# Kernel tuning notes

Measured on AMD Instinct MI355X. Metric: run time of the kernel, lower is better.

The kernel has to match this reference:

```python
import jax, jax.numpy as jnp
import numpy as np

TAU = 1.0
EPS = 1e-30
LN_EPS = 1e-5


def setup_inputs() -> dict:
    key = jax.random.key(0)
    ks = jax.random.split(key, 5)
    N, E, D_in, D_out = 50000, 800000, 128, 128
    x = jax.random.normal(ks[0], (N, D_in), dtype=jnp.float32)
    edge_src = jax.random.randint(ks[1], (E,), 0, N, dtype=jnp.int64)
    edge_dst = jax.random.randint(ks[2], (E,), 0, N, dtype=jnp.int64)
    W = jax.random.normal(ks[3], (2 * D_in, D_out), dtype=jnp.float32) * (1.0 / np.sqrt(2 * D_in))
    b = jnp.zeros((D_out,), dtype=jnp.float32)
    gamma = jnp.ones((D_out,), dtype=jnp.float32)
    beta = jnp.zeros((D_out,), dtype=jnp.float32)
    return {"x": x, "edge_src": edge_src, "edge_dst": edge_dst, "W": W, "b": b, "gamma": gamma, "beta": beta}


def _scatter_logsumexp(src, index, dim_size):
    # src: [E, D] gathered neighbor features, index: [E] target node ids
    scaled = src.astype(jnp.float32) / TAU
    mx = jax.ops.segment_max(scaled, index, num_segments=dim_size)  # [N, D], -inf for empty
    exp_val = jnp.exp(scaled - mx[index])                            # [E, D]
    sum_exp = jax.ops.segment_sum(exp_val, index, num_segments=dim_size)  # [N, D]
    out = TAU * (mx + jnp.log(jnp.maximum(sum_exp, EPS)))
    deg = jax.ops.segment_sum(jnp.ones_like(index, dtype=jnp.int32), index, num_segments=dim_size)
    return jnp.where((deg > 0)[:, None], out, 0.0)


def reference(x, edge_src, edge_dst, W, b, gamma, beta):
    N = x.shape[0]
    src_feat = x[edge_src]                                  # [E, D] gather
    agg = _scatter_logsumexp(src_feat, edge_dst, N)         # [N, D]
    h = jnp.concatenate([x, agg], axis=-1) @ W + b          # [N, D_out]
    mean = jnp.mean(h, axis=-1, keepdims=True)
    var = jnp.var(h, axis=-1, keepdims=True)
    h = (h - mean) * jax.lax.rsqrt(var + LN_EPS) * gamma + beta
    return jax.nn.relu(h)
```

## Files before the change

### kernel.cpp

```cpp
#include <hip/hip_runtime.h>
#include <math.h>

#define D 128
#define EPS 1e-30f
#define LN_EPS 1e-5f

#define BINSHIFT 9
#define BINW 512
#define NBIN_MAX 128
#define P1_EPB 4096

typedef long long ll;
typedef __attribute__((ext_vector_type(8))) short short8;
typedef __attribute__((ext_vector_type(4))) float f32x4;

__device__ inline unsigned short f2bf(float f) {
    unsigned int u = __float_as_uint(f);
    u += 0x7FFF + ((u >> 16) & 1);
    return (unsigned short)(u >> 16);
}

__device__ inline float bf2f_lo(unsigned int w) { return __uint_as_float(w << 16); }
__device__ inline float bf2f_hi(unsigned int w) { return __uint_as_float(w & 0xFFFF0000u); }

__device__ inline bool idx_is_i64(const void* p, int n_nodes) {
    const ll* q = (const ll*)p;
    bool ok = true;
#pragma unroll
    for (int i = 0; i < 4; ++i) {
        ll v = q[i];
        if (v < 0 || v >= (ll)n_nodes) ok = false;
    }
    return ok;
}

__device__ inline int load_idx(const void* p, ll e, bool is64) {
    return is64 ? (int)((const ll*)p)[e] : ((const int*)p)[e];
}


__global__ __launch_bounds__(256) void k_prep(const float* __restrict__ x,
                                              unsigned short* __restrict__ A, int N) {
    int i = blockIdx.x * 256 + threadIdx.x;
    if (i >= N * 32) return;
    int n = i >> 5, c4 = i & 31;
    float4 v = *(const float4*)(x + (ll)n * D + c4 * 4);
    ushort4 o;
    o.x = f2bf(v.x); o.y = f2bf(v.y); o.z = f2bf(v.z); o.w = f2bf(v.w);
    *(ushort4*)(A + (ll)n * 256 + c4 * 4) = o;
}

__global__ __launch_bounds__(256) void k_wt(const float* __restrict__ W,
                                            unsigned short* __restrict__ WT) {
    int idx = blockIdx.x * 256 + threadIdx.x;
    int k = idx >> 7, n = idx & 127;
    WT[n * 256 + k] = f2bf(W[idx]);
}

__global__ __launch_bounds__(256) void k_pass1a(const void* __restrict__ edst,
                                                int* __restrict__ bincnt, int E, int N) {
    __shared__ int hist[NBIN_MAX];
    bool is64 = idx_is_i64(edst, N);
    int t = threadIdx.x;
    if (t < NBIN_MAX) hist[t] = 0;
    __syncthreads();
    ll base = (ll)blockIdx.x * P1_EPB;
    int cnt = (int)min((ll)P1_EPB, (ll)E - base);
    for (int i = t; i < cnt; i += 256) {
        int d = load_idx(edst, base + i, is64);
        atomicAdd(&hist[d >> BINSHIFT], 1);
    }
    __syncthreads();
    if (t < NBIN_MAX && hist[t]) atomicAdd(&bincnt[t], hist[t]);
}

__global__ __launch_bounds__(NBIN_MAX) void k_binscan(const int* __restrict__ bincnt,
                                                      int* __restrict__ pbase,
                                                      int* __restrict__ pcur,
                                                      int* __restrict__ off, int E, int N) {
    __shared__ int s[NBIN_MAX];
    int t = threadIdx.x;
    int v = bincnt[t];
    s[t] = v;
    __syncthreads();
    for (int o = 1; o < NBIN_MAX; o <<= 1) {
        int xv = (t >= o) ? s[t - o] : 0;
        __syncthreads();
        s[t] += xv;
        __syncthreads();
    }
    pbase[t] = s[t] - v;
    pcur[t]  = s[t] - v;
    if (t == NBIN_MAX - 1) { pbase[NBIN_MAX] = s[t]; off[N] = E; }
}

__global__ __launch_bounds__(256) void k_pass1b(const void* __restrict__ esrc,
                                                const void* __restrict__ edst,
                                                int* __restrict__ pcur,
                                                unsigned int* __restrict__ pairs,
                                                int E, int N) {
    __shared__ unsigned int sp[P1_EPB];
    __shared__ int hist[NBIN_MAX];
    __shared__ int curs[NBIN_MAX];
    bool is64s = idx_is_i64(esrc, N);
    bool is64d = idx_is_i64(edst, N);
    int t = threadIdx.x;
    if (t < NBIN_MAX) hist[t] = 0;
    __syncthreads();
    ll base = (ll)blockIdx.x * P1_EPB;
    int cnt = (int)min((ll)P1_EPB, (ll)E - base);
    for (int i = t; i < cnt; i += 256) {
        unsigned int s = (unsigned int)load_idx(esrc, base + i, is64s);
        unsigned int d = (unsigned int)load_idx(edst, base + i, is64d);
        sp[i] = (d << 16) | s;
        atomicAdd(&hist[d >> BINSHIFT], 1);
    }
    __syncthreads();
    if (t < NBIN_MAX) curs[t] = hist[t] ? atomicAdd(&pcur[t], hist[t]) : 0;
    __syncthreads();
    for (int i = t; i < cnt; i += 256) {
        unsigned int p = sp[i];
        int b = p >> (16 + BINSHIFT);
        int pos = atomicAdd(&curs[b], 1);
        pairs[pos] = p;
    }
}

__global__ __launch_bounds__(256) void k_pass2(const unsigned int* __restrict__ pairs,
                                               const int* __restrict__ pbase,
                                               int* __restrict__ off,
                                               unsigned short* __restrict__ bucket, int N) {
    __shared__ int dhist[BINW];
    __shared__ int dcur[BINW];
    __shared__ int ssum[256];
    int b = blockIdx.x, t = threadIdx.x;
    int p0 = pbase[b], p1 = pbase[b + 1];
    int n0 = b << BINSHIFT;
    for (int j = t; j < BINW; j += 256) dhist[j] = 0;
    __syncthreads();
    for (int i = p0 + t; i < p1; i += 256)
        atomicAdd(&dhist[(pairs[i] >> 16) & (BINW - 1)], 1);
    __syncthreads();
    int h0 = dhist[2 * t], h1 = dhist[2 * t + 1];
    int loc = h0 + h1;
    ssum[t] = loc;
    __syncthreads();
    for (int o = 1; o < 256; o <<= 1) {
        int xv = (t >= o) ? ssum[t - o] : 0;
        __syncthreads();
        ssum[t] += xv;
        __syncthreads();
    }
    int ex = ssum[t] - loc;
    dcur[2 * t]     = ex;
    dcur[2 * t + 1] = ex + h0;
    __syncthreads();
    int lim = min(BINW, N - n0);
    for (int j = t; j < lim; j += 256) off[n0 + j] = p0 + dcur[j];
    __syncthreads();
    for (int i = p0 + t; i < p1; i += 256) {
        unsigned int p = pairs[i];
        int dl = (p >> 16) & (BINW - 1);
        int pos = p0 + atomicAdd(&dcur[dl], 1);
        bucket[pos] = (unsigned short)(p & 0xFFFFu);
    }
}

__global__ __launch_bounds__(256) void k_aggregate(const int* __restrict__ off,
                                                   const unsigned short* __restrict__ bucket,
                                                   unsigned short* __restrict__ A, int N) {
    int w = threadIdx.x >> 6, lane = threadIdx.x & 63;
    int n = blockIdx.x * 4 + w;
    if (n >= N) return;
    int start = off[n], end = off[n + 1];
    int sub = lane >> 4, c16 = lane & 15;
    float acc[8];
#pragma unroll
    for (int j = 0; j < 8; ++j) acc[j] = 0.f;
    for (int e = start + sub; e < end; e += 4) {
        int src = bucket[e];
        uint4 v = *(const uint4*)(A + (ll)src * 256 + c16 * 8);
        acc[0] += __expf(bf2f_lo(v.x)); acc[1] += __expf(bf2f_hi(v.x));
        acc[2] += __expf(bf2f_lo(v.y)); acc[3] += __expf(bf2f_hi(v.y));
        acc[4] += __expf(bf2f_lo(v.z)); acc[5] += __expf(bf2f_hi(v.z));
        acc[6] += __expf(bf2f_lo(v.w)); acc[7] += __expf(bf2f_hi(v.w));
    }
#pragma unroll
    for (int j = 0; j < 8; ++j) {
        acc[j] += __shfl_xor(acc[j], 16, 64);
        acc[j] += __shfl_xor(acc[j], 32, 64);
    }
    if (sub == 0) {
        int dg = end - start;
        unsigned int o[4];
#pragma unroll
        for (int k = 0; k < 4; ++k) {
            float a0 = (dg > 0) ? __logf(fmaxf(acc[2 * k],     EPS)) : 0.f;
            float a1 = (dg > 0) ? __logf(fmaxf(acc[2 * k + 1], EPS)) : 0.f;
            o[k] = (unsigned int)f2bf(a0) | ((unsigned int)f2bf(a1) << 16);
        }
        *(uint4*)(A + (ll)n * 256 + 128 + c16 * 8) = make_uint4(o[0], o[1], o[2], o[3]);
    }
}

__global__ __launch_bounds__(256) void k_gemm_mfma(
        const unsigned short* __restrict__ A,
        const unsigned short* __restrict__ WT,
        const float* __restrict__ bias,
        const float* __restrict__ gamma,
        const float* __restrict__ beta,
        float* __restrict__ out, int N) {
    __shared__ unsigned char sA[64 * 512];
    __shared__ float2 sPart[2][64];
    int t = threadIdx.x;
    int l = t & 63, w = t >> 6;
    int wr = w >> 1, wc = w & 1;
    int n0 = blockIdx.x * 64;

    const uint4* gA = (const uint4*)(A + (ll)n0 * 256);
#pragma unroll
    for (int i = 0; i < 8; ++i) {
        int c = i * 256 + t;
        int row = c >> 5, cc = c & 31;
        uint4 v = make_uint4(0u, 0u, 0u, 0u);
        if (n0 + row < N) v = gA[row * 32 + cc];
        *(uint4*)(sA + row * 512 + ((cc * 16) ^ ((row & 7) << 4))) = v;
    }
    __syncthreads();

    f32x4 acc[2][4];
#pragma unroll
    for (int m = 0; m < 2; ++m)
#pragma unroll
        for (int n = 0; n < 4; ++n) acc[m][n] = (f32x4){0.f, 0.f, 0.f, 0.f};

    const int lr = l & 15, lk = l >> 4;
    const int aswz = (lr & 7) << 4;
    const unsigned short* wbase = WT + (wc * 64 + lr) * 256 + lk * 8;

#pragma unroll
    for (int ks = 0; ks < 8; ++ks) {
        short8 a[2], b[4];
#pragma unroll
        for (int m = 0; m < 2; ++m) {
            int arow = wr * 32 + m * 16 + lr;
            a[m] = *(const short8*)(sA + arow * 512 + ((ks * 64 + lk * 16) ^ aswz));
        }
#pragma unroll
        for (int n = 0; n < 4; ++n)
            b[n] = *(const short8*)(wbase + n * 16 * 256 + ks * 32);
#pragma unroll
        for (int m = 0; m < 2; ++m)
#pragma unroll
            for (int n = 0; n < 4; ++n)
                acc[m][n] = __builtin_amdgcn_mfma_f32_16x16x32_bf16(a[m], b[n], acc[m][n], 0, 0, 0);
    }

    const int col_base = wc * 64 + lr;
    float bn[4], gn[4], ben[4];
#pragma unroll
    for (int n = 0; n < 4; ++n) {
        int col = col_base + n * 16;
        bn[n] = bias[col]; gn[n] = gamma[col]; ben[n] = beta[col];
    }
#pragma unroll
    for (int m = 0; m < 2; ++m) {
#pragma unroll
        for (int r = 0; r < 4; ++r) {
            float s = 0.f, q = 0.f;
#pragma unroll
            for (int n = 0; n < 4; ++n) {
                float v = acc[m][n][r] + bn[n];
                acc[m][n][r] = v;
                s += v; q += v * v;
            }
#pragma unroll
            for (int o = 1; o < 16; o <<= 1) {
                s += __shfl_xor(s, o, 64);
                q += __shfl_xor(q, o, 64);
            }
            if (lr == 0) {
                int rowl = wr * 32 + m * 16 + lk * 4 + r;
                sPart[wc][rowl] = make_float2(s, q);
            }
        }
    }
    __syncthreads();
#pragma unroll
    for (int m = 0; m < 2; ++m) {
#pragma unroll
        for (int r = 0; r < 4; ++r) {
            int rowl = wr * 32 + m * 16 + lk * 4 + r;
            float2 p0 = sPart[0][rowl], p1 = sPart[1][rowl];
            float ssum = p0.x + p1.x, qsum = p0.y + p1.y;
            float mean = ssum * (1.f / 128.f);
            float var  = qsum * (1.f / 128.f) - mean * mean;
            float rstd = rsqrtf(var + LN_EPS);
            int grow = n0 + rowl;
            if (grow < N) {
                float* op = out + (ll)grow * 128;
#pragma unroll
                for (int n = 0; n < 4; ++n) {
                    float y = (acc[m][n][r] - mean) * rstd * gn[n] + ben[n];
                    op[col_base + n * 16] = fmaxf(y, 0.f);
                }
            }
        }
    }
}


__global__ __launch_bounds__(256) void k_hist(const void* __restrict__ edst,
                                              int* __restrict__ deg, int E, int N) {
    bool is64 = idx_is_i64(edst, N);
    int i = blockIdx.x * 256 + threadIdx.x;
    if (i < E) atomicAdd(&deg[load_idx(edst, i, is64)], 1);
}

__global__ __launch_bounds__(256) void k_scanA(const int* __restrict__ deg,
                                               int* __restrict__ off,
                                               int* __restrict__ bsum, int N) {
    __shared__ int s[256];
    int b = blockIdx.x, t = threadIdx.x;
    int base = b * 1024 + t * 4;
    int v0 = 0, v1 = 0, v2 = 0, v3 = 0;
    if (base + 0 < N) v0 = deg[base + 0];
    if (base + 1 < N) v1 = deg[base + 1];
    if (base + 2 < N) v2 = deg[base + 2];
    if (base + 3 < N) v3 = deg[base + 3];
    int loc = v0 + v1 + v2 + v3;
    s[t] = loc;
    __syncthreads();
    for (int o = 1; o < 256; o <<= 1) {
        int xv = (t >= o) ? s[t - o] : 0;
        __syncthreads();
        s[t] += xv;
        __syncthreads();
    }
    int run = s[t] - loc;
    if (t == 255) bsum[b] = s[255];
    if (base + 0 < N) off[base + 0] = run; run += v0;
    if (base + 1 < N) off[base + 1] = run; run += v1;
    if (base + 2 < N) off[base + 2] = run; run += v2;
    if (base + 3 < N) off[base + 3] = run;
}

__global__ __launch_bounds__(256) void k_scanB(const int* __restrict__ bsum,
                                               int* __restrict__ bbase, int NB) {
    __shared__ int s[256];
    int t = threadIdx.x;
    int v = (t < NB) ? bsum[t] : 0;
    s[t] = v;
    __syncthreads();
    for (int o = 1; o < 256; o <<= 1) {
        int xv = (t >= o) ? s[t - o] : 0;
        __syncthreads();
        s[t] += xv;
        __syncthreads();
    }
    if (t < NB) bbase[t] = s[t] - v;
}

__global__ __launch_bounds__(256) void k_scanC(int* __restrict__ off,
                                               int* __restrict__ cur,
                                               const int* __restrict__ bbase, int N, int E) {
    int b = blockIdx.x, t = threadIdx.x;
    int add = bbase[b];
    int base = b * 1024 + t * 4;
#pragma unroll
    for (int i = 0; i < 4; ++i) {
        int idx = base + i;
        if (idx < N) {
            int o = off[idx] + add;
            off[idx] = o;
            cur[idx] = o;
        }
    }
    if (b == 0 && t == 0) off[N] = E;
}

__global__ __launch_bounds__(256) void k_scatter32(const void* __restrict__ esrc,
                                                   const void* __restrict__ edst,
                                                   int* __restrict__ cur,
                                                   unsigned short* __restrict__ bucket,
                                                   int E, int N) {
    bool is64s = idx_is_i64(esrc, N);
    bool is64d = idx_is_i64(edst, N);
    int i = blockIdx.x * 256 + threadIdx.x;
    if (i < E) {
        int s = load_idx(esrc, i, is64s);
        int d = load_idx(edst, i, is64d);
        int pos = atomicAdd(&cur[d], 1);
        bucket[pos] = (unsigned short)s;
    }
}


__global__ __launch_bounds__(256) void scatter_expsum(
        const float* __restrict__ x, const void* __restrict__ esrc_raw,
        const void* __restrict__ edst_raw, float* __restrict__ sumexp,
        int* __restrict__ deg, int E, int N) {
    ll tid = (ll)blockIdx.x * blockDim.x + threadIdx.x;
    ll total = (ll)E * 32;
    if (tid >= total) return;
    bool is64 = idx_is_i64(esrc_raw, N);
    ll e = tid >> 5;
    int q = (int)(tid & 31);
    int s = load_idx(esrc_raw, e, is64);
    int d = load_idx(edst_raw, e, is64);
    const float4 v = *reinterpret_cast<const float4*>(x + (ll)s * D + q * 4);
    float* outp = sumexp + (ll)d * D + q * 4;
    atomicAdd(outp + 0, expf(v.x));
    atomicAdd(outp + 1, expf(v.y));
    atomicAdd(outp + 2, expf(v.z));
    atomicAdd(outp + 3, expf(v.w));
    if (q == 0) atomicAdd(deg + d, 1);
}

__global__ __launch_bounds__(128) void gemm_ln_relu_fb(
        const float* __restrict__ x, const float* __restrict__ sumexp,
        const int* __restrict__ deg, const float* __restrict__ W,
        const float* __restrict__ bias, const float* __restrict__ gamma,
        const float* __restrict__ beta, float* __restrict__ out) {
    const int n = blockIdx.x;
    const int t = threadIdx.x;
    __shared__ float v[2 * D];
    __shared__ float s_sum[2], s_sq[2];
    v[t] = x[(ll)n * D + t];
    float se = sumexp[(ll)n * D + t];
    v[D + t] = (deg[n] > 0) ? logf(fmaxf(se, EPS)) : 0.0f;
    __syncthreads();
    float acc = bias[t];
#pragma unroll 8
    for (int k = 0; k < 2 * D; ++k) acc += v[k] * W[k * D + t];
    float sum = acc, sq = acc * acc;
#pragma unroll
    for (int o = 32; o > 0; o >>= 1) {
        sum += __shfl_xor(sum, o, 64);
        sq  += __shfl_xor(sq, o, 64);
    }
    int w = t >> 6;
    if ((t & 63) == 0) { s_sum[w] = sum; s_sq[w] = sq; }
    __syncthreads();
    float mean = (s_sum[0] + s_sum[1]) * (1.0f / D);
    float var  = (s_sq[0] + s_sq[1]) * (1.0f / D) - mean * mean;
    float r = rsqrtf(var + LN_EPS);
    float y = (acc - mean) * r * gamma[t] + beta[t];
    out[(ll)n * D + t] = fmaxf(y, 0.0f);
}

__global__ __launch_bounds__(128) void k_aggregate_mid(const float* __restrict__ x,
                                                       const unsigned short* __restrict__ bucket,
                                                       const int* __restrict__ off,
                                                       unsigned short* __restrict__ A, int N) {
    int n = blockIdx.x, t = threadIdx.x;
    int start = __builtin_amdgcn_readfirstlane(off[n]);
    int end   = __builtin_amdgcn_readfirstlane(off[n + 1]);
    float acc = 0.f;
    for (int e = start; e < end; ++e) {
        int s0 = bucket[e];
        acc += __expf(x[(ll)s0 * D + t]);
    }
    float agg = (end > start) ? __logf(fmaxf(acc, EPS)) : 0.f;
    A[(ll)n * 256 + t]       = f2bf(x[(ll)n * D + t]);
    A[(ll)n * 256 + 128 + t] = f2bf(agg);
}


extern "C" void kernel_launch(void* const* d_in, const int* in_sizes, int n_in,
                              void* d_out, int out_size, void* d_ws, size_t ws_size,
                              hipStream_t stream) {
    const float* x     = (const float*)d_in[0];
    const void*  esrc  = d_in[1];
    const void*  edst  = d_in[2];
    const float* W     = (const float*)d_in[3];
    const float* bias  = (const float*)d_in[4];
    const float* gamma = (const float*)d_in[5];
    const float* beta  = (const float*)d_in[6];

    const int E = in_sizes[1];
    const int N = in_sizes[0] / D;
    float* out = (float*)d_out;
    unsigned short* A = (unsigned short*)d_out;

    size_t need_fast = ((size_t)(N + 1) + 128 + 129 + 128 + (size_t)E) * 4
                     + (size_t)E * 2 + 2 + 65536;
    const int NB = (N + 1023) / 1024;
    size_t need_mid = ((size_t)3 * N + 1 + 512 + 16384) * 4 + (size_t)E * 2 + 2;

    if (N <= 65536 && ws_size >= need_fast) {
        int* off            = (int*)d_ws;
        int* bincnt         = off + (N + 1);
        int* pbase          = bincnt + 128;
        int* pcur           = pbase + 129;
        unsigned int* pairs = (unsigned int*)(pcur + 128);
        unsigned short* bucket = (unsigned short*)(pairs + E);
        unsigned short* wt  = (unsigned short*)((char*)(bucket + E) + (((size_t)(bucket + E)) & 2 ? 2 : 0));

        const int NBIN = (N + BINW - 1) >> BINSHIFT;
        const int EB = (E + P1_EPB - 1) / P1_EPB;

        hipMemsetAsync(bincnt, 0, 128 * sizeof(int), stream);
        k_prep<<<(N * 32 + 255) / 256, 256, 0, stream>>>(x, A, N);
        k_wt<<<128, 256, 0, stream>>>(W, wt);
        k_pass1a<<<EB, 256, 0, stream>>>(edst, bincnt, E, N);
        k_binscan<<<1, NBIN_MAX, 0, stream>>>(bincnt, pbase, pcur, off, E, N);
        k_pass1b<<<EB, 256, 0, stream>>>(esrc, edst, pcur, pairs, E, N);
        k_pass2<<<NBIN, 256, 0, stream>>>(pairs, pbase, off, bucket, N);
        k_aggregate<<<(N + 3) / 4, 256, 0, stream>>>(off, bucket, A, N);
        k_gemm_mfma<<<(N + 63) / 64, 256, 0, stream>>>(A, wt, bias, gamma, beta, out, N);
    } else if (N <= 65536 && ws_size >= need_mid && NB <= 256) {
        int* deg    = (int*)d_ws;
        int* off    = deg + N;
        int* cur    = off + (N + 1);
        int* bsum   = cur + N;
        int* bbase  = bsum + 256;
        unsigned short* wt = (unsigned short*)(bbase + 256);
        unsigned short* bucket = wt + 32768;

        hipMemsetAsync(deg, 0, (size_t)N * sizeof(int), stream);
        int eb = (E + 255) / 256;
        k_wt<<<128, 256, 0, stream>>>(W, wt);
        k_hist<<<eb, 256, 0, stream>>>(edst, deg, E, N);
        k_scanA<<<NB, 256, 0, stream>>>(deg, off, bsum, N);
        k_scanB<<<1, 256, 0, stream>>>(bsum, bbase, NB);
        k_scanC<<<NB, 256, 0, stream>>>(off, cur, bbase, N, E);
        k_scatter32<<<eb, 256, 0, stream>>>(esrc, edst, cur, bucket, E, N);
        k_aggregate_mid<<<N, 128, 0, stream>>>(x, bucket, off, A, N);
        k_gemm_mfma<<<(N + 63) / 64, 256, 0, stream>>>(A, wt, bias, gamma, beta, out, N);
    } else {
        float* sumexp = out;
        int* deg = (int*)d_ws;
        hipMemsetAsync(sumexp, 0, (size_t)N * D * sizeof(float), stream);
        hipMemsetAsync(deg, 0, (size_t)N * sizeof(int), stream);
        ll total = (ll)E * 32;
        int blocks = (int)((total + 255) / 256);
        scatter_expsum<<<blocks, 256, 0, stream>>>(x, esrc, edst, sumexp, deg, E, N);
        gemm_ln_relu_fb<<<N, D, 0, stream>>>(x, sumexp, deg, W, bias, gamma, beta, out);
    }
}
```

Before: 136.0 us.

## Fuse prep, weight transpose and bin histogram into one setup kernel; unroll aggregation

Merges the x-to-bf16 conversion, the W transpose and the per-block destination-bin histogram into a single launch. The histogram now writes per-block counts that k_binscan sums, which removes the memset and the global atomics. The aggregation loop is also unrolled by two so that two gathers are in flight at once. This cuts launch overhead and adds latency hiding, at the cost of a serial loop over EB rows inside the single-block binscan.

```diff
diff --git a/kernel.cpp b/kernel.cpp
--- a/kernel.cpp
+++ b/kernel.cpp
@@ -39,48 +39,55 @@
 }
 
 
-__global__ __launch_bounds__(256) void k_prep(const float* __restrict__ x,
-                                              unsigned short* __restrict__ A, int N) {
-    int i = blockIdx.x * 256 + threadIdx.x;
-    if (i >= N * 32) return;
-    int n = i >> 5, c4 = i & 31;
-    float4 v = *(const float4*)(x + (ll)n * D + c4 * 4);
-    ushort4 o;
-    o.x = f2bf(v.x); o.y = f2bf(v.y); o.z = f2bf(v.z); o.w = f2bf(v.w);
-    *(ushort4*)(A + (ll)n * 256 + c4 * 4) = o;
-}
-
-__global__ __launch_bounds__(256) void k_wt(const float* __restrict__ W,
-                                            unsigned short* __restrict__ WT) {
-    int idx = blockIdx.x * 256 + threadIdx.x;
-    int k = idx >> 7, n = idx & 127;
-    WT[n * 256 + k] = f2bf(W[idx]);
-}
-
-__global__ __launch_bounds__(256) void k_pass1a(const void* __restrict__ edst,
-                                                int* __restrict__ bincnt, int E, int N) {
+__global__ __launch_bounds__(256) void k_setup(const float* __restrict__ x,
+                                               unsigned short* __restrict__ A,
+                                               const float* __restrict__ W,
+                                               unsigned short* __restrict__ WT,
+                                               const void* __restrict__ edst,
+                                               int* __restrict__ bhist,
+                                               int N, int E, int PREP_B, int WT_B) {
     __shared__ int hist[NBIN_MAX];
+    int b = blockIdx.x, t = threadIdx.x;
+    if (b < PREP_B) {
+        int i = b * 256 + t;
+        if (i < N * 32) {
+            int n = i >> 5, c4 = i & 31;
+            float4 v = *(const float4*)(x + (ll)n * D + c4 * 4);
+            ushort4 o;
+            o.x = f2bf(v.x); o.y = f2bf(v.y); o.z = f2bf(v.z); o.w = f2bf(v.w);
+            *(ushort4*)(A + (ll)n * 256 + c4 * 4) = o;
+        }
+        return;
+    }
+    b -= PREP_B;
+    if (b < WT_B) {
+        int idx = b * 256 + t;
+        int k = idx >> 7, n = idx & 127;
+        WT[n * 256 + k] = f2bf(W[idx]);
+        return;
+    }
+    b -= WT_B;
+    if (t < NBIN_MAX) hist[t] = 0;
+    __syncthreads();
     bool is64 = idx_is_i64(edst, N);
-    int t = threadIdx.x;
-    if (t < NBIN_MAX) hist[t] = 0;
-    __syncthreads();
-    ll base = (ll)blockIdx.x * P1_EPB;
+    ll base = (ll)b * P1_EPB;
     int cnt = (int)min((ll)P1_EPB, (ll)E - base);
     for (int i = t; i < cnt; i += 256) {
         int d = load_idx(edst, base + i, is64);
         atomicAdd(&hist[d >> BINSHIFT], 1);
     }
     __syncthreads();
-    if (t < NBIN_MAX && hist[t]) atomicAdd(&bincnt[t], hist[t]);
-}
-
-__global__ __launch_bounds__(NBIN_MAX) void k_binscan(const int* __restrict__ bincnt,
+    if (t < NBIN_MAX) bhist[b * NBIN_MAX + t] = hist[t];
+}
+
+__global__ __launch_bounds__(NBIN_MAX) void k_binscan(const int* __restrict__ bhist, int EB,
                                                       int* __restrict__ pbase,
                                                       int* __restrict__ pcur,
                                                       int* __restrict__ off, int E, int N) {
     __shared__ int s[NBIN_MAX];
     int t = threadIdx.x;
-    int v = bincnt[t];
+    int v = 0;
+    for (int i = 0; i < EB; ++i) v += bhist[i * NBIN_MAX + t];
     s[t] = v;
     __syncthreads();
     for (int o = 1; o < NBIN_MAX; o <<= 1) {
@@ -174,16 +181,32 @@
     if (n >= N) return;
     int start = off[n], end = off[n + 1];
     int sub = lane >> 4, c16 = lane & 15;
+    const uint4* A4 = (const uint4*)A;
     float acc[8];
 #pragma unroll
     for (int j = 0; j < 8; ++j) acc[j] = 0.f;
-    for (int e = start + sub; e < end; e += 4) {
-        int src = bucket[e];
-        uint4 v = *(const uint4*)(A + (ll)src * 256 + c16 * 8);
-        acc[0] += __expf(bf2f_lo(v.x)); acc[1] += __expf(bf2f_hi(v.x));
-        acc[2] += __expf(bf2f_lo(v.y)); acc[3] += __expf(bf2f_hi(v.y));
-        acc[4] += __expf(bf2f_lo(v.z)); acc[5] += __expf(bf2f_hi(v.z));
-        acc[6] += __expf(bf2f_lo(v.w)); acc[7] += __expf(bf2f_hi(v.w));
+    int e = start + sub;
+    for (; e + 4 < end; e += 8) {
+        int s0 = bucket[e];
+        int s1 = bucket[e + 4];
+        uint4 v0 = A4[(ll)s0 * 32 + c16];
+        uint4 v1 = A4[(ll)s1 * 32 + c16];
+        acc[0] += __expf(bf2f_lo(v0.x)); acc[1] += __expf(bf2f_hi(v0.x));
+        acc[2] += __expf(bf2f_lo(v0.y)); acc[3] += __expf(bf2f_hi(v0.y));
+        acc[4] += __expf(bf2f_lo(v0.z)); acc[5] += __expf(bf2f_hi(v0.z));
+        acc[6] += __expf(bf2f_lo(v0.w)); acc[7] += __expf(bf2f_hi(v0.w));
+        acc[0] += __expf(bf2f_lo(v1.x)); acc[1] += __expf(bf2f_hi(v1.x));
+        acc[2] += __expf(bf2f_lo(v1.y)); acc[3] += __expf(bf2f_hi(v1.y));
+        acc[4] += __expf(bf2f_lo(v1.z)); acc[5] += __expf(bf2f_hi(v1.z));
+        acc[6] += __expf(bf2f_lo(v1.w)); acc[7] += __expf(bf2f_hi(v1.w));
+    }
+    if (e < end) {
+        int s0 = bucket[e];
+        uint4 v0 = A4[(ll)s0 * 32 + c16];
+        acc[0] += __expf(bf2f_lo(v0.x)); acc[1] += __expf(bf2f_hi(v0.x));
+        acc[2] += __expf(bf2f_lo(v0.y)); acc[3] += __expf(bf2f_hi(v0.y));
+        acc[4] += __expf(bf2f_lo(v0.z)); acc[5] += __expf(bf2f_hi(v0.z));
+        acc[6] += __expf(bf2f_lo(v0.w)); acc[7] += __expf(bf2f_hi(v0.w));
     }
 #pragma unroll
     for (int j = 0; j < 8; ++j) {
@@ -310,6 +333,13 @@
 }
 
 
+__global__ __launch_bounds__(256) void k_wt(const float* __restrict__ W,
+                                            unsigned short* __restrict__ WT) {
+    int idx = blockIdx.x * 256 + threadIdx.x;
+    int k = idx >> 7, n = idx & 127;
+    WT[n * 256 + k] = f2bf(W[idx]);
+}
+
 __global__ __launch_bounds__(256) void k_hist(const void* __restrict__ edst,
                                               int* __restrict__ deg, int E, int N) {
     bool is64 = idx_is_i64(edst, N);
@@ -393,6 +423,23 @@
         int pos = atomicAdd(&cur[d], 1);
         bucket[pos] = (unsigned short)s;
     }
+}
+
+__global__ __launch_bounds__(128) void k_aggregate_mid(const float* __restrict__ x,
+                                                       const unsigned short* __restrict__ bucket,
+                                                       const int* __restrict__ off,
+                                                       unsigned short* __restrict__ A, int N) {
+    int n = blockIdx.x, t = threadIdx.x;
+    int start = __builtin_amdgcn_readfirstlane(off[n]);
+    int end   = __builtin_amdgcn_readfirstlane(off[n + 1]);
+    float acc = 0.f;
+    for (int e = start; e < end; ++e) {
+        int s0 = bucket[e];
+        acc += __expf(x[(ll)s0 * D + t]);
+    }
+    float agg = (end > start) ? __logf(fmaxf(acc, EPS)) : 0.f;
+    A[(ll)n * 256 + t]       = f2bf(x[(ll)n * D + t]);
+    A[(ll)n * 256 + 128 + t] = f2bf(agg);
 }
 
 
@@ -449,23 +496,6 @@
     out[(ll)n * D + t] = fmaxf(y, 0.0f);
 }
 
-__global__ __launch_bounds__(128) void k_aggregate_mid(const float* __restrict__ x,
-                                                       const unsigned short* __restrict__ bucket,
-                                                       const int* __restrict__ off,
-                                                       unsigned short* __restrict__ A, int N) {
-    int n = blockIdx.x, t = threadIdx.x;
-    int start = __builtin_amdgcn_readfirstlane(off[n]);
-    int end   = __builtin_amdgcn_readfirstlane(off[n + 1]);
-    float acc = 0.f;
-    for (int e = start; e < end; ++e) {
-        int s0 = bucket[e];
-        acc += __expf(x[(ll)s0 * D + t]);
-    }
-    float agg = (end > start) ? __logf(fmaxf(acc, EPS)) : 0.f;
-    A[(ll)n * 256 + t]       = f2bf(x[(ll)n * D + t]);
-    A[(ll)n * 256 + 128 + t] = f2bf(agg);
-}
-
 
 extern "C" void kernel_launch(void* const* d_in, const int* in_sizes, int n_in,
                               void* d_out, int out_size, void* d_ws, size_t ws_size,
@@ -483,28 +513,26 @@
     float* out = (float*)d_out;
     unsigned short* A = (unsigned short*)d_out;
 
-    size_t need_fast = ((size_t)(N + 1) + 128 + 129 + 128 + (size_t)E) * 4
+    const int EB = (E + P1_EPB - 1) / P1_EPB;
+    const int PREP_B = (N * 32 + 255) / 256;
+    const int NBIN = (N + BINW - 1) >> BINSHIFT;
+
+    size_t need_fast = ((size_t)(N + 1) + 129 + 128 + (size_t)EB * NBIN_MAX + (size_t)E) * 4
                      + (size_t)E * 2 + 2 + 65536;
     const int NB = (N + 1023) / 1024;
     size_t need_mid = ((size_t)3 * N + 1 + 512 + 16384) * 4 + (size_t)E * 2 + 2;
 
     if (N <= 65536 && ws_size >= need_fast) {
         int* off            = (int*)d_ws;
-        int* bincnt         = off + (N + 1);
-        int* pbase          = bincnt + 128;
+        int* pbase          = off + (N + 1);
         int* pcur           = pbase + 129;
-        unsigned int* pairs = (unsigned int*)(pcur + 128);
+        int* bhist          = pcur + 128;
+        unsigned int* pairs = (unsigned int*)(bhist + (size_t)EB * NBIN_MAX);
         unsigned short* bucket = (unsigned short*)(pairs + E);
         unsigned short* wt  = (unsigned short*)((char*)(bucket + E) + (((size_t)(bucket + E)) & 2 ? 2 : 0));
 
-        const int NBIN = (N + BINW - 1) >> BINSHIFT;
-        const int EB = (E + P1_EPB - 1) / P1_EPB;
-
-        hipMemsetAsync(bincnt, 0, 128 * sizeof(int), stream);
-        k_prep<<<(N * 32 + 255) / 256, 256, 0, stream>>>(x, A, N);
-        k_wt<<<128, 256, 0, stream>>>(W, wt);
-        k_pass1a<<<EB, 256, 0, stream>>>(edst, bincnt, E, N);
-        k_binscan<<<1, NBIN_MAX, 0, stream>>>(bincnt, pbase, pcur, off, E, N);
+        k_setup<<<PREP_B + 128 + EB, 256, 0, stream>>>(x, A, W, wt, edst, bhist, N, E, PREP_B, 128);
+        k_binscan<<<1, NBIN_MAX, 0, stream>>>(bhist, EB, pbase, pcur, off, E, N);
         k_pass1b<<<EB, 256, 0, stream>>>(esrc, edst, pcur, pairs, E, N);
         k_pass2<<<NBIN, 256, 0, stream>>>(pairs, pbase, off, bucket, N);
         k_aggregate<<<(N + 3) / 4, 256, 0, stream>>>(off, bucket, A, N);
```

Measured after the change: 141.1 us. 3.8% more time.
